# Optimization experiments

Hardware: AMD Instinct MI355X
Metric: run time of the kernel (lower is better)

The kernel has to match this reference:

```python
import jax, jax.numpy as jnp
import numpy as np

B, T, D = 2048, 200, 64
H1, H2 = 80, 40
NEG_INF = -4294967295.0  # -(2**32) + 1 as in original


def setup_inputs() -> dict:
    key0 = jax.random.key(0)
    ks = jax.random.split(key0, 10)
    din_dim = 4 * D
    inp = {
        "query": jax.random.normal(ks[0], (B, D), dtype=jnp.float32),
        "key": jax.random.normal(ks[1], (B, T, D), dtype=jnp.float32),
        "mask": jax.random.randint(ks[2], (B,), 1, T + 1, dtype=jnp.int32),
        # MLP params (Dense 4D->80->40->1, use_bias=True)
        "W1": jax.random.normal(ks[3], (din_dim, H1), dtype=jnp.float32) / np.sqrt(din_dim),
        "b1": jnp.zeros((H1,), dtype=jnp.float32),
        "W2": jax.random.normal(ks[4], (H1, H2), dtype=jnp.float32) / np.sqrt(H1),
        "b2": jnp.zeros((H2,), dtype=jnp.float32),
        "W3": jax.random.normal(ks[5], (H2, 1), dtype=jnp.float32) / np.sqrt(H2),
        "b3": jnp.zeros((1,), dtype=jnp.float32),
    }
    return inp


def reference(query, key, mask, W1, b1, W2, b2, W3, b3):
    b, t, d = key.shape
    q = query[:, None, :]                      # [B,1,D]
    q_tile = jnp.broadcast_to(q, (b, t, d))    # [B,T,D]
    din_all = jnp.concatenate([q_tile, key, q_tile - key, q_tile * key], axis=-1)  # [B,T,4D]
    h = jax.nn.sigmoid(jnp.einsum("btf,fh->bth", din_all, W1) + b1)
    h = jax.nn.sigmoid(jnp.einsum("bth,hg->btg", h, W2) + b2)
    score = (jnp.einsum("btg,go->bto", h, W3) + b3)[..., 0]  # [B,T]
    key_mask = jnp.arange(t)[None, :] < mask[:, None]        # [B,T]
    score = jnp.where(key_mask, score, NEG_INF)
    score = score / jnp.asarray(d, score.dtype) ** 0.5
    attn = jax.nn.softmax(score, axis=-1)                    # [B,T]
    out = jnp.einsum("bt,btd->bd", attn, key)                # [B,D] (squeezed)
    return out
```

## Files before the change

kernel.cpp:

```cpp
#include <hip/hip_runtime.h>
#include <math.h>

#define B_  2048
#define T_  200
#define D_  64
#define H1_ 80
#define H2_ 40

#define WSTR 104
#define HSTR 104

#define WS_A    0
#define WS_C    10240
#define WS_W2T  20480
#define WS_ACT  30464

typedef __bf16 bf16x8 __attribute__((ext_vector_type(8)));
typedef float  f32x4  __attribute__((ext_vector_type(4)));

__device__ __forceinline__ float sigmoidf_(float x) {
    return __builtin_amdgcn_rcpf(1.0f + __expf(-x));
}

__global__ __launch_bounds__(256)
void prep_kernel(const float* __restrict__ W1, const float* __restrict__ W2,
                 void* __restrict__ ws)
{
    __bf16* A    = (__bf16*)((char*)ws + WS_A);
    __bf16* C    = (__bf16*)((char*)ws + WS_C);
    __bf16* W2Tp = (__bf16*)((char*)ws + WS_W2T);
    float*  acT  = (float*)((char*)ws + WS_ACT);
    const int e0 = blockIdx.x * 256 + threadIdx.x;

    for (int e = e0; e < H1_ * D_; e += 2048) {
        int h = e >> 6, f = e & 63;
        float wb = W1[(64  + f) * H1_ + h];
        float wc = W1[(128 + f) * H1_ + h];
        float wd = W1[(192 + f) * H1_ + h];
        float wa = W1[f * H1_ + h];
        A[e]   = (__bf16)(wb - wc);
        C[e]   = (__bf16)wd;
        acT[e] = wa + wc;
    }
    for (int e = e0; e < 48 * WSTR; e += 2048) {
        int g = e / WSTR, h = e - g * WSTR;
        W2Tp[e] = (g < H2_ && h < H1_) ? (__bf16)W2[h * H2_ + g] : (__bf16)0.0f;
    }
}

__global__ __launch_bounds__(256, 2)
void attn_din17(const float* __restrict__ query,
                const float* __restrict__ key,
                const int*   __restrict__ mask,
                const float* __restrict__ b1,
                const float* __restrict__ b2,
                const float* __restrict__ W3,
                const float* __restrict__ b3,
                const void*  __restrict__ ws,
                float* __restrict__ out)
{
    __shared__ __align__(16) __bf16 s_h1[4][32 * HSTR];
    __shared__ __align__(16) float  s_q[4][D_];
    __shared__ float s_base[4][H1_];
    __shared__ float s_part[4][D_];

    const int tid  = threadIdx.x;
    const int lane = tid & 63;
    const int w    = tid >> 6;
    const int c16  = lane & 15;
    const int g16  = lane >> 4;
    const int b    = blockIdx.x * 4 + w;

    const int   mv     = mask[b];
    const int   npairs = (mv + 31) >> 5;
    const float b3v    = b3[0];
    const float* kb = key + (size_t)b * T_ * D_;

    const __bf16* wsA   = (const __bf16*)((const char*)ws + WS_A);
    const __bf16* wsC   = (const __bf16*)((const char*)ws + WS_C);
    const __bf16* wsW2T = (const __bf16*)((const char*)ws + WS_W2T);
    const float*  wsacT = (const float*) ((const char*)ws + WS_ACT);

    float qv = query[b * D_ + lane];
    float4 uA0, uA1, uA2, uA3, uB0, uB1, uB2, uB3;
    {
        const float* krA = kb + (size_t)c16 * D_ + g16 * 8;
        const float* krB = kb + (size_t)(16 + c16) * D_ + g16 * 8;
        uA0 = *(const float4*)(krA);      uA1 = *(const float4*)(krA + 4);
        uA2 = *(const float4*)(krA + 32); uA3 = *(const float4*)(krA + 36);
        uB0 = *(const float4*)(krB);      uB1 = *(const float4*)(krB + 4);
        uB2 = *(const float4*)(krB + 32); uB3 = *(const float4*)(krB + 36);
    }
    s_q[w][lane] = qv;

    bf16x8 bw[3][3];
    #pragma unroll
    for (int nt = 0; nt < 3; ++nt)
        #pragma unroll
        for (int ks = 0; ks < 3; ++ks)
            bw[nt][ks] = *(const bf16x8*)&wsW2T[(nt * 16 + c16) * WSTR + ks * 32 + g16 * 8];

    float b2c[3], w3c[3];
    #pragma unroll
    for (int nt = 0; nt < 3; ++nt) {
        int g = nt * 16 + c16;
        b2c[nt] = (g < H2_) ? b2[g] : 0.0f;
        w3c[nt] = (g < H2_) ? W3[g] : 0.0f;
    }

    {
        float a0 = b1[lane], a1 = 0.0f, a2 = 0.0f, a3 = 0.0f;
        const f32x4* row = (const f32x4*)&wsacT[lane * D_];
        #pragma unroll
        for (int f4 = 0; f4 < 16; ++f4) {
            f32x4 v  = row[f4];
            f32x4 q4 = *(const f32x4*)&s_q[w][f4 * 4];
            a0 = fmaf(q4[0], v[0], a0);
            a1 = fmaf(q4[1], v[1], a1);
            a2 = fmaf(q4[2], v[2], a2);
            a3 = fmaf(q4[3], v[3], a3);
        }
        s_base[w][lane] = (a0 + a1) + (a2 + a3);
    }
    if (lane < 16) {
        int h = 64 + lane;
        float a0 = b1[h], a1 = 0.0f, a2 = 0.0f, a3 = 0.0f;
        const f32x4* row = (const f32x4*)&wsacT[h * D_];
        #pragma unroll
        for (int f4 = 0; f4 < 16; ++f4) {
            f32x4 v  = row[f4];
            f32x4 q4 = *(const f32x4*)&s_q[w][f4 * 4];
            a0 = fmaf(q4[0], v[0], a0);
            a1 = fmaf(q4[1], v[1], a1);
            a2 = fmaf(q4[2], v[2], a2);
            a3 = fmaf(q4[3], v[3], a3);
        }
        s_base[w][h] = (a0 + a1) + (a2 + a3);
    }

    bf16x8 bv[5][2];
    #pragma unroll
    for (int nt = 0; nt < 5; ++nt)
        #pragma unroll
        for (int ks = 0; ks < 2; ++ks) {
            int off = (nt * 16 + c16) * D_ + ks * 32 + g16 * 8;
            bf16x8 a8 = *(const bf16x8*)&wsA[off];
            bf16x8 c8 = *(const bf16x8*)&wsC[off];
            f32x4 q0 = *(const f32x4*)&s_q[w][ks * 32 + g16 * 8];
            f32x4 q1 = *(const f32x4*)&s_q[w][ks * 32 + g16 * 8 + 4];
            bf16x8 v8;
            v8[0] = (__bf16)((float)a8[0] + q0[0] * (float)c8[0]);
            v8[1] = (__bf16)((float)a8[1] + q0[1] * (float)c8[1]);
            v8[2] = (__bf16)((float)a8[2] + q0[2] * (float)c8[2]);
            v8[3] = (__bf16)((float)a8[3] + q0[3] * (float)c8[3]);
            v8[4] = (__bf16)((float)a8[4] + q1[0] * (float)c8[4]);
            v8[5] = (__bf16)((float)a8[5] + q1[1] * (float)c8[5]);
            v8[6] = (__bf16)((float)a8[6] + q1[2] * (float)c8[6]);
            v8[7] = (__bf16)((float)a8[7] + q1[3] * (float)c8[7]);
            bv[nt][ks] = v8;
        }

    {
        int row = lane & 31, c0 = 80 + (lane >> 5) * 8;
        *(uint4*)&s_h1[w][row * HSTR + c0] = make_uint4(0u, 0u, 0u, 0u);
    }

    float base_c[5];
    #pragma unroll
    for (int nt = 0; nt < 5; ++nt) base_c[nt] = s_base[w][nt * 16 + c16];
    __bf16* myh = &s_h1[w][0];

    float o00,o01,o02,o03,o04,o05,o06,o07,o08,o09,o10,o11,o12,o13,o14,o15;
    o00=o01=o02=o03=o04=o05=o06=o07=o08=o09=o10=o11=o12=o13=o14=o15=0.0f;
    float l_run = 0.0f;

    for (int pp = 0; pp < npairs; ++pp) {
        bf16x8 afA0, afA1, afB0, afB1;
        afA0[0]=(__bf16)uA0.x; afA0[1]=(__bf16)uA0.y; afA0[2]=(__bf16)uA0.z; afA0[3]=(__bf16)uA0.w;
        afA0[4]=(__bf16)uA1.x; afA0[5]=(__bf16)uA1.y; afA0[6]=(__bf16)uA1.z; afA0[7]=(__bf16)uA1.w;
        afA1[0]=(__bf16)uA2.x; afA1[1]=(__bf16)uA2.y; afA1[2]=(__bf16)uA2.z; afA1[3]=(__bf16)uA2.w;
        afA1[4]=(__bf16)uA3.x; afA1[5]=(__bf16)uA3.y; afA1[6]=(__bf16)uA3.z; afA1[7]=(__bf16)uA3.w;
        afB0[0]=(__bf16)uB0.x; afB0[1]=(__bf16)uB0.y; afB0[2]=(__bf16)uB0.z; afB0[3]=(__bf16)uB0.w;
        afB0[4]=(__bf16)uB1.x; afB0[5]=(__bf16)uB1.y; afB0[6]=(__bf16)uB1.z; afB0[7]=(__bf16)uB1.w;
        afB1[0]=(__bf16)uB2.x; afB1[1]=(__bf16)uB2.y; afB1[2]=(__bf16)uB2.z; afB1[3]=(__bf16)uB2.w;
        afB1[4]=(__bf16)uB3.x; afB1[5]=(__bf16)uB3.y; afB1[6]=(__bf16)uB3.z; afB1[7]=(__bf16)uB3.w;

        if (pp + 1 < npairs) {
            int trA = (pp + 1) * 32 + c16;
            int trB = trA + 16;
            const float* krA = kb + (size_t)((trA < T_) ? trA : (T_ - 1)) * D_ + g16 * 8;
            const float* krB = kb + (size_t)((trB < T_) ? trB : (T_ - 1)) * D_ + g16 * 8;
            uA0 = *(const float4*)(krA);      uA1 = *(const float4*)(krA + 4);
            uA2 = *(const float4*)(krA + 32); uA3 = *(const float4*)(krA + 36);
            uB0 = *(const float4*)(krB);      uB1 = *(const float4*)(krB + 4);
            uB2 = *(const float4*)(krB + 32); uB3 = *(const float4*)(krB + 36);
        }

        #pragma unroll
        for (int nt = 0; nt < 5; ++nt) {
            float bb = base_c[nt];
            f32x4 cA = { bb, bb, bb, bb };
            cA = __builtin_amdgcn_mfma_f32_16x16x32_bf16(afA0, bv[nt][0], cA, 0, 0, 0);
            cA = __builtin_amdgcn_mfma_f32_16x16x32_bf16(afA1, bv[nt][1], cA, 0, 0, 0);
            f32x4 cB = { bb, bb, bb, bb };
            cB = __builtin_amdgcn_mfma_f32_16x16x32_bf16(afB0, bv[nt][0], cB, 0, 0, 0);
            cB = __builtin_amdgcn_mfma_f32_16x16x32_bf16(afB1, bv[nt][1], cB, 0, 0, 0);
            #pragma unroll
            for (int r = 0; r < 4; ++r) {
                myh[(g16 * 4 + r) * HSTR + nt * 16 + c16]      = (__bf16)sigmoidf_(cA[r]);
                myh[(16 + g16 * 4 + r) * HSTR + nt * 16 + c16] = (__bf16)sigmoidf_(cB[r]);
            }
        }

        bf16x8 a2A0 = *(const bf16x8*)&myh[c16 * HSTR + g16 * 8];
        bf16x8 a2A1 = *(const bf16x8*)&myh[c16 * HSTR + 32 + g16 * 8];
        bf16x8 a2A2 = *(const bf16x8*)&myh[c16 * HSTR + 64 + g16 * 8];
        bf16x8 a2B0 = *(const bf16x8*)&myh[(16 + c16) * HSTR + g16 * 8];
        bf16x8 a2B1 = *(const bf16x8*)&myh[(16 + c16) * HSTR + 32 + g16 * 8];
        bf16x8 a2B2 = *(const bf16x8*)&myh[(16 + c16) * HSTR + 64 + g16 * 8];
        f32x4 acc2A[3], acc2B[3];
        #pragma unroll
        for (int nt = 0; nt < 3; ++nt) {
            float bb = b2c[nt];
            f32x4 cA = { bb, bb, bb, bb };
            cA = __builtin_amdgcn_mfma_f32_16x16x32_bf16(a2A0, bw[nt][0], cA, 0, 0, 0);
            cA = __builtin_amdgcn_mfma_f32_16x16x32_bf16(a2A1, bw[nt][1], cA, 0, 0, 0);
            cA = __builtin_amdgcn_mfma_f32_16x16x32_bf16(a2A2, bw[nt][2], cA, 0, 0, 0);
            acc2A[nt] = cA;
            f32x4 cB = { bb, bb, bb, bb };
            cB = __builtin_amdgcn_mfma_f32_16x16x32_bf16(a2B0, bw[nt][0], cB, 0, 0, 0);
            cB = __builtin_amdgcn_mfma_f32_16x16x32_bf16(a2B1, bw[nt][1], cB, 0, 0, 0);
            cB = __builtin_amdgcn_mfma_f32_16x16x32_bf16(a2B2, bw[nt][2], cB, 0, 0, 0);
            acc2B[nt] = cB;
        }

        float redA[4], redB[4];
        #pragma unroll
        for (int r = 0; r < 4; ++r) {
            float pA = sigmoidf_(acc2A[0][r]) * w3c[0]
                     + sigmoidf_(acc2A[1][r]) * w3c[1]
                     + sigmoidf_(acc2A[2][r]) * w3c[2];
            float pB = sigmoidf_(acc2B[0][r]) * w3c[0]
                     + sigmoidf_(acc2B[1][r]) * w3c[1]
                     + sigmoidf_(acc2B[2][r]) * w3c[2];
            pA += __shfl_xor(pA, 1);  pB += __shfl_xor(pB, 1);
            pA += __shfl_xor(pA, 2);  pB += __shfl_xor(pB, 2);
            pA += __shfl_xor(pA, 4);  pB += __shfl_xor(pB, 4);
            pA += __shfl_xor(pA, 8);  pB += __shfl_xor(pB, 8);
            redA[r] = pA;  redB[r] = pB;
        }

        const int srcLane = ((c16 >> 2) << 4) | c16;
        float sA = 0.0f, sB = 0.0f;
        #pragma unroll
        for (int r = 0; r < 4; ++r) {
            float tA = __shfl(redA[r], srcLane);
            float tB = __shfl(redB[r], srcLane);
            if ((c16 & 3) == r) { sA = tA; sB = tB; }
        }

        const int tb = pp * 32;
        int tA_ = tb + c16, tB_ = tb + 16 + c16;
        float pA = (tA_ < mv) ? __expf((sA + b3v) * 0.125f) : 0.0f;
        float pB = (tB_ < mv) ? __expf((sB + b3v) * 0.125f) : 0.0f;

        float psum = pA + pB;
        psum += __shfl_xor(psum, 1);
        psum += __shfl_xor(psum, 2);
        psum += __shfl_xor(psum, 4);
        psum += __shfl_xor(psum, 8);
        l_run += psum;

        o00 = fmaf(pB, (float)afB0[0], fmaf(pA, (float)afA0[0], o00));
        o01 = fmaf(pB, (float)afB0[1], fmaf(pA, (float)afA0[1], o01));
        o02 = fmaf(pB, (float)afB0[2], fmaf(pA, (float)afA0[2], o02));
        o03 = fmaf(pB, (float)afB0[3], fmaf(pA, (float)afA0[3], o03));
        o04 = fmaf(pB, (float)afB0[4], fmaf(pA, (float)afA0[4], o04));
        o05 = fmaf(pB, (float)afB0[5], fmaf(pA, (float)afA0[5], o05));
        o06 = fmaf(pB, (float)afB0[6], fmaf(pA, (float)afA0[6], o06));
        o07 = fmaf(pB, (float)afB0[7], fmaf(pA, (float)afA0[7], o07));
        o08 = fmaf(pB, (float)afB1[0], fmaf(pA, (float)afA1[0], o08));
        o09 = fmaf(pB, (float)afB1[1], fmaf(pA, (float)afA1[1], o09));
        o10 = fmaf(pB, (float)afB1[2], fmaf(pA, (float)afA1[2], o10));
        o11 = fmaf(pB, (float)afB1[3], fmaf(pA, (float)afA1[3], o11));
        o12 = fmaf(pB, (float)afB1[4], fmaf(pA, (float)afA1[4], o12));
        o13 = fmaf(pB, (float)afB1[5], fmaf(pA, (float)afA1[5], o13));
        o14 = fmaf(pB, (float)afB1[6], fmaf(pA, (float)afA1[6], o14));
        o15 = fmaf(pB, (float)afB1[7], fmaf(pA, (float)afA1[7], o15));
    }

    #define ORED(X) X += __shfl_xor(X,1); X += __shfl_xor(X,2); X += __shfl_xor(X,4); X += __shfl_xor(X,8);
    ORED(o00) ORED(o01) ORED(o02) ORED(o03) ORED(o04) ORED(o05) ORED(o06) ORED(o07)
    ORED(o08) ORED(o09) ORED(o10) ORED(o11) ORED(o12) ORED(o13) ORED(o14) ORED(o15)
    #undef ORED
    float inv_total = __builtin_amdgcn_rcpf(l_run);
    if (c16 == 0) {
        float* sp = &s_part[w][0];
        sp[g16 * 8 + 0] = o00;  sp[g16 * 8 + 1] = o01;
        sp[g16 * 8 + 2] = o02;  sp[g16 * 8 + 3] = o03;
        sp[g16 * 8 + 4] = o04;  sp[g16 * 8 + 5] = o05;
        sp[g16 * 8 + 6] = o06;  sp[g16 * 8 + 7] = o07;
        sp[32 + g16 * 8 + 0] = o08;  sp[32 + g16 * 8 + 1] = o09;
        sp[32 + g16 * 8 + 2] = o10;  sp[32 + g16 * 8 + 3] = o11;
        sp[32 + g16 * 8 + 4] = o12;  sp[32 + g16 * 8 + 5] = o13;
        sp[32 + g16 * 8 + 6] = o14;  sp[32 + g16 * 8 + 7] = o15;
    }
    asm volatile("s_waitcnt lgkmcnt(0)" ::: "memory");
    out[b * D_ + lane] = s_part[w][lane] * inv_total;
}

extern "C" void kernel_launch(void* const* d_in, const int* in_sizes, int n_in,
                              void* d_out, int out_size, void* d_ws, size_t ws_size,
                              hipStream_t stream)
{
    const float* query = (const float*)d_in[0];
    const float* key   = (const float*)d_in[1];
    const int*   mask  = (const int*)  d_in[2];
    const float* W1    = (const float*)d_in[3];
    const float* b1    = (const float*)d_in[4];
    const float* W2    = (const float*)d_in[5];
    const float* b2    = (const float*)d_in[6];
    const float* W3    = (const float*)d_in[7];
    const float* b3    = (const float*)d_in[8];
    float* out = (float*)d_out;

    prep_kernel<<<8, 256, 0, stream>>>(W1, W2, d_ws);
    attn_din17<<<512, 256, 0, stream>>>(query, key, mask, b1, b2, W3, b3, d_ws, out);
}
```

Measured before the change: 45.18 us.

## Keep layer-1 activations in registers via transposed MFMA and cross-lane shuffles

Swaps the MFMA operand order so each lane's layer-1 outputs are indexed by hidden unit instead of timestep. The sigmoid outputs are packed to bf16 pairs and rearranged with lane shuffles into the B operand of the layer-2 MFMA, so the shared-memory staging buffer and its LDS round-trip are no longer needed. The layer-3 reduction now uses two xor shuffles. This cuts LDS traffic and LDS size, at the cost of many extra shuffle instructions per 32-step chunk and higher register pressure.

```diff
diff --git a/kernel.cpp b/kernel.cpp
--- a/kernel.cpp
+++ b/kernel.cpp
@@ -8,7 +8,6 @@
 #define H2_ 40
 
 #define WSTR 104
-#define HSTR 104
 
 #define WS_A    0
 #define WS_C    10240
@@ -20,6 +19,12 @@
 
 __device__ __forceinline__ float sigmoidf_(float x) {
     return __builtin_amdgcn_rcpf(1.0f + __expf(-x));
+}
+__device__ __forceinline__ unsigned pk2_(float a, float b) {
+    __bf16 x = (__bf16)a, y = (__bf16)b;
+    unsigned short ux = __builtin_bit_cast(unsigned short, x);
+    unsigned short uy = __builtin_bit_cast(unsigned short, y);
+    return (unsigned)ux | ((unsigned)uy << 16);
 }
 
 __global__ __launch_bounds__(256)
@@ -49,7 +54,7 @@
 }
 
 __global__ __launch_bounds__(256, 2)
-void attn_din17(const float* __restrict__ query,
+void attn_din18(const float* __restrict__ query,
                 const float* __restrict__ key,
                 const int*   __restrict__ mask,
                 const float* __restrict__ b1,
@@ -59,8 +64,7 @@
                 const void*  __restrict__ ws,
                 float* __restrict__ out)
 {
-    __shared__ __align__(16) __bf16 s_h1[4][32 * HSTR];
-    __shared__ __align__(16) float  s_q[4][D_];
+    __shared__ __align__(16) float s_q[4][D_];
     __shared__ float s_base[4][H1_];
     __shared__ float s_part[4][D_];
 
@@ -100,13 +104,15 @@
         for (int ks = 0; ks < 3; ++ks)
             bw[nt][ks] = *(const bf16x8*)&wsW2T[(nt * 16 + c16) * WSTR + ks * 32 + g16 * 8];
 
-    float b2c[3], w3c[3];
+    float b2c[3][4], w3c[3][4];
     #pragma unroll
-    for (int nt = 0; nt < 3; ++nt) {
-        int g = nt * 16 + c16;
-        b2c[nt] = (g < H2_) ? b2[g] : 0.0f;
-        w3c[nt] = (g < H2_) ? W3[g] : 0.0f;
-    }
+    for (int nt = 0; nt < 3; ++nt)
+        #pragma unroll
+        for (int r = 0; r < 4; ++r) {
+            int g = nt * 16 + g16 * 4 + r;
+            b2c[nt][r] = (g < H2_) ? b2[g] : 0.0f;
+            w3c[nt][r] = (g < H2_) ? W3[g] : 0.0f;
+        }
 
     {
         float a0 = b1[lane], a1 = 0.0f, a2 = 0.0f, a3 = 0.0f;
@@ -140,10 +146,10 @@
 
     bf16x8 bv[5][2];
     #pragma unroll
-    for (int nt = 0; nt < 5; ++nt)
+    for (int mt = 0; mt < 5; ++mt)
         #pragma unroll
         for (int ks = 0; ks < 2; ++ks) {
-            int off = (nt * 16 + c16) * D_ + ks * 32 + g16 * 8;
+            int off = (mt * 16 + c16) * D_ + ks * 32 + g16 * 8;
             bf16x8 a8 = *(const bf16x8*)&wsA[off];
             bf16x8 c8 = *(const bf16x8*)&wsC[off];
             f32x4 q0 = *(const f32x4*)&s_q[w][ks * 32 + g16 * 8];
@@ -157,18 +163,19 @@
             v8[5] = (__bf16)((float)a8[5] + q1[1] * (float)c8[5]);
             v8[6] = (__bf16)((float)a8[6] + q1[2] * (float)c8[6]);
             v8[7] = (__bf16)((float)a8[7] + q1[3] * (float)c8[7]);
-            bv[nt][ks] = v8;
-        }
-
-    {
-        int row = lane & 31, c0 = 80 + (lane >> 5) * 8;
-        *(uint4*)&s_h1[w][row * HSTR + c0] = make_uint4(0u, 0u, 0u, 0u);
-    }
-
-    float base_c[5];
+            bv[mt][ks] = v8;
+        }
+
+    float base_c[5][4];
     #pragma unroll
-    for (int nt = 0; nt < 5; ++nt) base_c[nt] = s_base[w][nt * 16 + c16];
-    __bf16* myh = &s_h1[w][0];
+    for (int mt = 0; mt < 5; ++mt)
+        #pragma unroll
+        for (int r = 0; r < 4; ++r)
+            base_c[mt][r] = s_base[w][16 * mt + g16 * 4 + r];
+
+    const int  L0 = ((g16 & 1) << 5) + c16;
+    const int  L1 = L0 + 16;
+    const bool hi = (g16 >= 2);
 
     float o00,o01,o02,o03,o04,o05,o06,o07,o08,o09,o10,o11,o12,o13,o14,o15;
     o00=o01=o02=o03=o04=o05=o06=o07=o08=o09=o10=o11=o12=o13=o14=o15=0.0f;
@@ -196,73 +203,68 @@
             uB2 = *(const float4*)(krB + 32); uB3 = *(const float4*)(krB + 36);
         }
 
-        #pragma unroll
-        for (int nt = 0; nt < 5; ++nt) {
-            float bb = base_c[nt];
-            f32x4 cA = { bb, bb, bb, bb };
-            cA = __builtin_amdgcn_mfma_f32_16x16x32_bf16(afA0, bv[nt][0], cA, 0, 0, 0);
-            cA = __builtin_amdgcn_mfma_f32_16x16x32_bf16(afA1, bv[nt][1], cA, 0, 0, 0);
-            f32x4 cB = { bb, bb, bb, bb };
-            cB = __builtin_amdgcn_mfma_f32_16x16x32_bf16(afB0, bv[nt][0], cB, 0, 0, 0);
-            cB = __builtin_amdgcn_mfma_f32_16x16x32_bf16(afB1, bv[nt][1], cB, 0, 0, 0);
+        unsigned pkA[5][2], pkB[5][2];
+        #pragma unroll
+        for (int mt = 0; mt < 5; ++mt) {
+            f32x4 cA = { base_c[mt][0], base_c[mt][1], base_c[mt][2], base_c[mt][3] };
+            cA = __builtin_amdgcn_mfma_f32_16x16x32_bf16(bv[mt][0], afA0, cA, 0, 0, 0);
+            cA = __builtin_amdgcn_mfma_f32_16x16x32_bf16(bv[mt][1], afA1, cA, 0, 0, 0);
+            f32x4 cB = { base_c[mt][0], base_c[mt][1], base_c[mt][2], base_c[mt][3] };
+            cB = __builtin_amdgcn_mfma_f32_16x16x32_bf16(bv[mt][0], afB0, cB, 0, 0, 0);
+            cB = __builtin_amdgcn_mfma_f32_16x16x32_bf16(bv[mt][1], afB1, cB, 0, 0, 0);
+            pkA[mt][0] = pk2_(sigmoidf_(cA[0]), sigmoidf_(cA[1]));
+            pkA[mt][1] = pk2_(sigmoidf_(cA[2]), sigmoidf_(cA[3]));
+            pkB[mt][0] = pk2_(sigmoidf_(cB[0]), sigmoidf_(cB[1]));
+            pkB[mt][1] = pk2_(sigmoidf_(cB[2]), sigmoidf_(cB[3]));
+        }
+
+        float sA, sB;
+        #pragma unroll
+        for (int sub = 0; sub < 2; ++sub) {
+            unsigned w00,w01,w02,w03, w10,w11,w12,w13, w20,w21,w22,w23;
+            {
+                #define PKX(m,i) (sub ? pkB[m][i] : pkA[m][i])
+                unsigned a,bq;
+                a = __shfl(PKX(0,0), L0); bq = __shfl(PKX(1,0), L0); w00 = hi ? bq : a;
+                a = __shfl(PKX(0,1), L0); bq = __shfl(PKX(1,1), L0); w01 = hi ? bq : a;
+                a = __shfl(PKX(0,0), L1); bq = __shfl(PKX(1,0), L1); w02 = hi ? bq : a;
+                a = __shfl(PKX(0,1), L1); bq = __shfl(PKX(1,1), L1); w03 = hi ? bq : a;
+                a = __shfl(PKX(2,0), L0); bq = __shfl(PKX(3,0), L0); w10 = hi ? bq : a;
+                a = __shfl(PKX(2,1), L0); bq = __shfl(PKX(3,1), L0); w11 = hi ? bq : a;
+                a = __shfl(PKX(2,0), L1); bq = __shfl(PKX(3,0), L1); w12 = hi ? bq : a;
+                a = __shfl(PKX(2,1), L1); bq = __shfl(PKX(3,1), L1); w13 = hi ? bq : a;
+                a = __shfl(PKX(4,0), L0);                            w20 = hi ? 0u : a;
+                a = __shfl(PKX(4,1), L0);                            w21 = hi ? 0u : a;
+                a = __shfl(PKX(4,0), L1);                            w22 = hi ? 0u : a;
+                a = __shfl(PKX(4,1), L1);                            w23 = hi ? 0u : a;
+                #undef PKX
+            }
+            union { unsigned u[4]; bf16x8 v; } cv0, cv1, cv2;
+            cv0.u[0]=w00; cv0.u[1]=w01; cv0.u[2]=w02; cv0.u[3]=w03;
+            cv1.u[0]=w10; cv1.u[1]=w11; cv1.u[2]=w12; cv1.u[3]=w13;
+            cv2.u[0]=w20; cv2.u[1]=w21; cv2.u[2]=w22; cv2.u[3]=w23;
+
+            float partial = 0.0f;
             #pragma unroll
-            for (int r = 0; r < 4; ++r) {
-                myh[(g16 * 4 + r) * HSTR + nt * 16 + c16]      = (__bf16)sigmoidf_(cA[r]);
-                myh[(16 + g16 * 4 + r) * HSTR + nt * 16 + c16] = (__bf16)sigmoidf_(cB[r]);
+            for (int nt2 = 0; nt2 < 3; ++nt2) {
+                f32x4 c = { b2c[nt2][0], b2c[nt2][1], b2c[nt2][2], b2c[nt2][3] };
+                c = __builtin_amdgcn_mfma_f32_16x16x32_bf16(bw[nt2][0], cv0.v, c, 0, 0, 0);
+                c = __builtin_amdgcn_mfma_f32_16x16x32_bf16(bw[nt2][1], cv1.v, c, 0, 0, 0);
+                c = __builtin_amdgcn_mfma_f32_16x16x32_bf16(bw[nt2][2], cv2.v, c, 0, 0, 0);
+                partial += sigmoidf_(c[0]) * w3c[nt2][0];
+                partial += sigmoidf_(c[1]) * w3c[nt2][1];
+                partial += sigmoidf_(c[2]) * w3c[nt2][2];
+                partial += sigmoidf_(c[3]) * w3c[nt2][3];
             }
-        }
-
-        bf16x8 a2A0 = *(const bf16x8*)&myh[c16 * HSTR + g16 * 8];
-        bf16x8 a2A1 = *(const bf16x8*)&myh[c16 * HSTR + 32 + g16 * 8];
-        bf16x8 a2A2 = *(const bf16x8*)&myh[c16 * HSTR + 64 + g16 * 8];
-        bf16x8 a2B0 = *(const bf16x8*)&myh[(16 + c16) * HSTR + g16 * 8];
-        bf16x8 a2B1 = *(const bf16x8*)&myh[(16 + c16) * HSTR + 32 + g16 * 8];
-        bf16x8 a2B2 = *(const bf16x8*)&myh[(16 + c16) * HSTR + 64 + g16 * 8];
-        f32x4 acc2A[3], acc2B[3];
-        #pragma unroll
-        for (int nt = 0; nt < 3; ++nt) {
-            float bb = b2c[nt];
-            f32x4 cA = { bb, bb, bb, bb };
-            cA = __builtin_amdgcn_mfma_f32_16x16x32_bf16(a2A0, bw[nt][0], cA, 0, 0, 0);
-            cA = __builtin_amdgcn_mfma_f32_16x16x32_bf16(a2A1, bw[nt][1], cA, 0, 0, 0);
-            cA = __builtin_amdgcn_mfma_f32_16x16x32_bf16(a2A2, bw[nt][2], cA, 0, 0, 0);
-            acc2A[nt] = cA;
-            f32x4 cB = { bb, bb, bb, bb };
-            cB = __builtin_amdgcn_mfma_f32_16x16x32_bf16(a2B0, bw[nt][0], cB, 0, 0, 0);
-            cB = __builtin_amdgcn_mfma_f32_16x16x32_bf16(a2B1, bw[nt][1], cB, 0, 0, 0);
-            cB = __builtin_amdgcn_mfma_f32_16x16x32_bf16(a2B2, bw[nt][2], cB, 0, 0, 0);
-            acc2B[nt] = cB;
-        }
-
-        float redA[4], redB[4];
-        #pragma unroll
-        for (int r = 0; r < 4; ++r) {
-            float pA = sigmoidf_(acc2A[0][r]) * w3c[0]
-                     + sigmoidf_(acc2A[1][r]) * w3c[1]
-                     + sigmoidf_(acc2A[2][r]) * w3c[2];
-            float pB = sigmoidf_(acc2B[0][r]) * w3c[0]
-                     + sigmoidf_(acc2B[1][r]) * w3c[1]
-                     + sigmoidf_(acc2B[2][r]) * w3c[2];
-            pA += __shfl_xor(pA, 1);  pB += __shfl_xor(pB, 1);
-            pA += __shfl_xor(pA, 2);  pB += __shfl_xor(pB, 2);
-            pA += __shfl_xor(pA, 4);  pB += __shfl_xor(pB, 4);
-            pA += __shfl_xor(pA, 8);  pB += __shfl_xor(pB, 8);
-            redA[r] = pA;  redB[r] = pB;
-        }
-
-        const int srcLane = ((c16 >> 2) << 4) | c16;
-        float sA = 0.0f, sB = 0.0f;
-        #pragma unroll
-        for (int r = 0; r < 4; ++r) {
-            float tA = __shfl(redA[r], srcLane);
-            float tB = __shfl(redB[r], srcLane);
-            if ((c16 & 3) == r) { sA = tA; sB = tB; }
+            partial += __shfl_xor(partial, 16);
+            partial += __shfl_xor(partial, 32);
+            float sc = (partial + b3v) * 0.125f;
+            if (sub == 0) sA = sc; else sB = sc;
         }
 
         const int tb = pp * 32;
-        int tA_ = tb + c16, tB_ = tb + 16 + c16;
-        float pA = (tA_ < mv) ? __expf((sA + b3v) * 0.125f) : 0.0f;
-        float pB = (tB_ < mv) ? __expf((sB + b3v) * 0.125f) : 0.0f;
+        float pA = (tb + c16 < mv)      ? __expf(sA) : 0.0f;
+        float pB = (tb + 16 + c16 < mv) ? __expf(sB) : 0.0f;
 
         float psum = pA + pB;
         psum += __shfl_xor(psum, 1);
@@ -325,5 +327,5 @@
     float* out = (float*)d_out;
 
     prep_kernel<<<8, 256, 0, stream>>>(W1, W2, d_ws);
-    attn_din17<<<512, 256, 0, stream>>>(query, key, mask, b1, b2, W3, b3, d_ws, out);
-}
+    attn_din18<<<512, 256, 0, stream>>>(query, key, mask, b1, b2, W3, b3, d_ws, out);
+}
```

Result: faster. 43.74 us (-3.2%).
